# Kernel tuning notes

Measured on AMD Instinct MI355X. Metric: run time of the kernel, lower is better.

The kernel has to match this reference:

```python
import jax, jax.numpy as jnp
import numpy as np

LOG2PI = float(np.log(2.0 * np.pi))


def setup_inputs() -> dict:
    key = jax.random.key(0)
    k1, k2, k3 = jax.random.split(key, 3)
    N, D = 2048, 64
    z = jax.random.normal(k1, (N, D), dtype=jnp.float32)
    z_mean = jax.random.normal(k2, (N, D), dtype=jnp.float32)
    z_log_squared_scale = jax.random.normal(k3, (N, D), dtype=jnp.float32)
    return {"z": z, "z_mean": z_mean, "z_log_squared_scale": z_log_squared_scale}


def gaussian_log_density(samples, mean, log_var):
    # log N(samples; mean, exp(log_var)), elementwise per dim
    inv_var = jnp.exp(-log_var)
    diff = samples - mean
    return -0.5 * (diff * diff * inv_var + log_var + LOG2PI)


def reference(z, z_mean, z_log_squared_scale):
    # Pairwise log q(z_i | x_j) per latent dim: [N, N, D]
    log_qz_prob = gaussian_log_density(
        z[:, None, :], z_mean[None, :, :], z_log_squared_scale[None, :, :]
    )
    # sum_d logsumexp_j  -> log prod_d q(z_d)
    log_qz_product = jnp.sum(jax.scipy.special.logsumexp(log_qz_prob, axis=1), axis=1)
    # logsumexp_j sum_d  -> log q(z)
    log_qz = jax.scipy.special.logsumexp(jnp.sum(log_qz_prob, axis=2), axis=1)
    return jnp.mean(log_qz_product - log_qz)
```

## Files before the change

kernel.cpp:

```cpp
#include <hip/hip_runtime.h>
#include <hip/hip_fp16.h>
#include <math.h>
#include <stdint.h>

#define LOG2E  1.44269504088896340736f
#define LN2    0.69314718055994530942f
#define LOG2PI 1.8378770664093453f

#define NN 2048
#define DD 64

#define BIAS_F   16252928.0f
#define KBIT     2205910303u
#define CLAMP_LO 8388608.0f
#define CLAMP_HI 16777215.0f

#define C1250H 0x64E264E2u
#define KK16   0x63DC63DCu
#define SHL5   0x00050005u

typedef short          bf16x8 __attribute__((ext_vector_type(8)));
typedef float          f32x16 __attribute__((ext_vector_type(16)));

union PkU { uint32_t u; __half h[2]; };

__device__ __forceinline__ float fexp2(float x) { return __builtin_amdgcn_exp2f(x); }
__device__ __forceinline__ float flog2(float x) { return __builtin_amdgcn_logf(x); }
__device__ __forceinline__ unsigned short f2bf(float f) {
    uint32_t u = __float_as_uint(f);
    u += 0x7FFFu + ((u >> 16) & 1u);
    return (unsigned short)(u >> 16);
}
__device__ __forceinline__ float ubf(unsigned short s) {
    return __uint_as_float((uint32_t)s << 16);
}
__device__ __forceinline__ uint32_t bfpack(float a, float b) {
    return (uint32_t)f2bf(a) | ((uint32_t)f2bf(b) << 16);
}
__device__ __forceinline__ uint32_t h1(float x) {
    return (uint32_t)__half_as_ushort(__float2half_rn(x));
}
__device__ __forceinline__ uint32_t hdup(float x) { uint32_t t = h1(x); return t | (t << 16); }
__device__ __forceinline__ uint32_t hpack(float a, float b) { return h1(a) | (h1(b) << 16); }

__device__ __forceinline__ uint32_t pk_fma(uint32_t a, uint32_t b, uint32_t c) {
    uint32_t d;
    asm("v_pk_fma_f16 %0, %1, %2, %3" : "=v"(d) : "v"(a), "v"(b), "v"(c));
    return d;
}
__device__ __forceinline__ uint32_t pk_nfma(uint32_t a, uint32_t b, uint32_t c) {
    uint32_t d;
    asm("v_pk_fma_f16 %0, %1, %2, %3 neg_lo:[1,0,0] neg_hi:[1,0,0]"
        : "=v"(d) : "v"(a), "v"(b), "v"(c));
    return d;
}
__device__ __forceinline__ uint32_t pk_max(uint32_t a, uint32_t b) {
    uint32_t d;
    asm("v_pk_max_f16 %0, %1, %2" : "=v"(d) : "v"(a), "v"(b));
    return d;
}
__device__ __forceinline__ uint32_t pk_addf(uint32_t a, uint32_t b) {
    uint32_t d;
    asm("v_pk_add_f16 %0, %1, %2" : "=v"(d) : "v"(a), "v"(b));
    return d;
}
__device__ __forceinline__ uint32_t pk_shl(uint32_t a, uint32_t sh) {
    uint32_t d;
    asm("v_pk_lshlrev_b16 %0, %1, %2" : "=v"(d) : "v"(sh), "v"(a));
    return d;
}
__device__ __forceinline__ uint32_t pk_addu(uint32_t a, uint32_t b) {
    uint32_t d;
    asm("v_pk_add_u16 %0, %1, %2" : "=v"(d) : "v"(a), "v"(b));
    return d;
}

__global__ __launch_bounds__(256) void k1(
    const float* __restrict__ z, const float* __restrict__ zm,
    const float* __restrict__ zlv,
    uint4* __restrict__ smC4,
    uint32_t* __restrict__ pqfH, uint32_t* __restrict__ pqfL,
    uint32_t* __restrict__ zfH, uint32_t* __restrict__ zfL,
    float* __restrict__ CjS, uint32_t* __restrict__ zpkT)
{
    __shared__ float L[32][65];
    int tid = threadIdx.x, lane = tid & 63, row = tid >> 6;

    if (blockIdx.x < 128) {
        int jb = blockIdx.x * 16;
        #pragma unroll
        for (int c = 0; c < 4; ++c) {
            int j   = jb + c * 4 + row;
            int idx = j * DD + lane;
            float mean = zm[idx], lv = zlv[idx];
            float p   = -0.72134752f * fexp2(-lv * LOG2E);
            float q   = -2.0f * mean * p;
            float c22 = -0.72134752f * (lv + LOG2PI);
            float sp  = 5.65685424f * __builtin_sqrtf(-p);
            float msp = -mean * sp;
            float Cp  = fmaf(32.0f, c22, 1952.0f);
            smC4[idx] = make_uint4(hdup(sp), hdup(msp), hdup(Cp), 0u);
            unsigned short hp = f2bf(p), hq = f2bf(q);
            pqfH[idx] = (uint32_t)hp | ((uint32_t)hq << 16);
            pqfL[idx] = bfpack(p - ubf(hp), q - ubf(hq));
            float t = fmaf(mean * mean, p, c22);
            #pragma unroll
            for (int off = 32; off; off >>= 1) t += __shfl_xor(t, off, 64);
            if (lane == 0) CjS[j] = fmaf(t + 64.0f, 65536.0f, BIAS_F);
        }
    } else {
        int ib = (blockIdx.x - 128) * 32;
        #pragma unroll
        for (int c = 0; c < 8; ++c) {
            int il  = c * 4 + row;
            int idx = (ib + il) * DD + lane;
            float zv = z[idx];
            L[il][lane] = zv;
            float z2 = zv * zv;
            unsigned short hz2 = f2bf(z2), hz = f2bf(zv);
            zfH[idx] = (uint32_t)hz2 | ((uint32_t)hz << 16);
            zfL[idx] = bfpack(z2 - ubf(hz2), zv - ubf(hz));
        }
        __syncthreads();
        #pragma unroll
        for (int k = 0; k < 4; ++k) {
            int e = k * 256 + tid;
            int u = e & 7, d = (e >> 3) & 63, itl = e >> 9;
            float za = L[itl * 16 + 2 * u][d];
            float zb = L[itl * 16 + 2 * u + 1][d];
            zpkT[((ib >> 4) + itl) * 512 + d * 8 + u] = hpack(za, zb);
        }
    }
}

__global__ __launch_bounds__(256) void kw(
    const uint4* __restrict__ smC4, const uint32_t* __restrict__ zpkT,
    const uint32_t* __restrict__ zfH, const uint32_t* __restrict__ zfL,
    const uint32_t* __restrict__ pqfH, const uint32_t* __restrict__ pqfL,
    const float* __restrict__ CjS,
    __half* __restrict__ sums, float* __restrict__ k2part)
{
    __shared__ float shbuf[4096];
    int tid = threadIdx.x, lane = tid & 63, w = tid >> 6;

    if (blockIdx.x < 1024) {
        float (*sm)[16][64] = (float (*)[16][64])shbuf;
        int it = blockIdx.x >> 3, jsl = blockIdx.x & 7;
        int j0 = jsl * 256 + w * 64;

        uint32_t zpk[8], acc[8];
        #pragma unroll
        for (int u = 0; u < 8; ++u) {
            zpk[u] = zpkT[it * 512 + lane * 8 + u];
            acc[u] = 0u;
        }
        uint32_t kk = KK16, sh5 = SHL5, clf = C1250H;
        asm volatile("" : "+v"(kk), "+v"(sh5), "+v"(clf));

        const uint4* sp = smC4 + (size_t)j0 * DD + lane;
        #pragma unroll 4
        for (int jj = 0; jj < 64; ++jj) {
            uint4 v = sp[(size_t)jj * DD];
            #pragma unroll
            for (int u = 0; u < 8; ++u) {
                uint32_t wp = pk_fma(zpk[u], v.x, v.y);
                uint32_t y  = pk_nfma(wp, wp, v.z);
                y = pk_max(y, clf);
                uint32_t e = pk_addu(pk_shl(y, sh5), kk);
                acc[u] = pk_addf(acc[u], e);
            }
        }

        #pragma unroll
        for (int u = 0; u < 8; ++u) {
            PkU a; a.u = acc[u];
            sm[w][2 * u][lane]     = __half2float(a.h[0]);
            sm[w][2 * u + 1][lane] = __half2float(a.h[1]);
        }
        __syncthreads();
        #pragma unroll
        for (int k = 0; k < 4; ++k) {
            int e = k * 256 + tid;
            int il = e >> 6, d = e & 63;
            float v2 = sm[0][il][d] + sm[1][il][d] + sm[2][il][d] + sm[3][il][d];
            sums[((size_t)jsl * NN + it * 16 + il) * DD + d] =
                __float2half_rn(v2 * 0.0625f);
        }
    } else {
        float* cjsL = shbuf;
        for (int t = tid; t < NN; t += 256) cjsL[t] = CjS[t];
        __syncthreads();

        int gid = (blockIdx.x - 1024) * 4 + w;
        int it = gid >> 5, jg = gid & 31;
        int l31 = lane & 31, h = lane >> 5;

        const char* zbH = (const char*)zfH + (size_t)(it * 32 + l31) * 256 + h * 16;
        const char* zbL = (const char*)zfL + (size_t)(it * 32 + l31) * 256 + h * 16;
        bf16x8 BH[8], BL[8];
        #pragma unroll
        for (int kc = 0; kc < 8; ++kc) {
            BH[kc] = *(const bf16x8*)(zbH + kc * 32);
            BL[kc] = *(const bf16x8*)(zbL + kc * 32);
        }

        float isum = 0.0f;
        #pragma unroll
        for (int t4 = 0; t4 < 2; ++t4) {
            int jt = jg * 2 + t4;
            const char* abH = (const char*)pqfH + (size_t)(jt * 32 + l31) * 256 + h * 16;
            const char* abL = (const char*)pqfL + (size_t)(jt * 32 + l31) * 256 + h * 16;
            f32x16 acc;
            #pragma unroll
            for (int r = 0; r < 16; ++r) acc[r] = 0.0f;
            #pragma unroll
            for (int kc = 0; kc < 8; ++kc) {
                bf16x8 AH = *(const bf16x8*)(abH + kc * 32);
                bf16x8 AL = *(const bf16x8*)(abL + kc * 32);
                acc = __builtin_amdgcn_mfma_f32_32x32x16_bf16(AH, BH[kc], acc, 0, 0, 0);
                acc = __builtin_amdgcn_mfma_f32_32x32x16_bf16(AH, BL[kc], acc, 0, 0, 0);
                acc = __builtin_amdgcn_mfma_f32_32x32x16_bf16(AL, BH[kc], acc, 0, 0, 0);
            }
            #pragma unroll
            for (int r = 0; r < 16; ++r) {
                int R = (r & 3) + 8 * (r >> 2) + 4 * h;
                float y = fmaf(acc[r], 65536.0f, cjsL[jt * 32 + R]);
                y = fminf(fmaxf(y, CLAMP_LO), CLAMP_HI);
                isum += __uint_as_float((__float_as_uint(y) << 7) + KBIT);
            }
        }
        isum += __shfl_xor(isum, 32, 64);
        if (lane < 32) k2part[(size_t)jg * NN + it * 32 + l31] = isum;
    }
}

__global__ __launch_bounds__(256) void k5(
    const __half* __restrict__ sums, const float* __restrict__ k2part,
    float* __restrict__ diff)
{
    int lane = threadIdx.x & 63, w = threadIdx.x >> 6;
    int i = blockIdx.x * 4 + w;

    float tot = 0.0f;
    #pragma unroll
    for (int q = 0; q < 8; ++q)
        tot += __half2float(sums[((size_t)q * NN + i) * DD + lane]);
    float t = flog2(tot);
    #pragma unroll
    for (int off = 32; off; off >>= 1) t += __shfl_xor(t, off, 64);

    float s2 = (lane < 32) ? k2part[(size_t)lane * NN + i] : 0.0f;
    #pragma unroll
    for (int off = 32; off; off >>= 1) s2 += __shfl_xor(s2, off, 64);

    if (lane == 0) diff[i] = LN2 * (t - flog2(s2) - 128.0f);
}

__global__ __launch_bounds__(256) void k6(
    const float* __restrict__ diff, float* __restrict__ out)
{
    __shared__ float red[256];
    int tid = threadIdx.x;
    float t = 0.0f;
    for (int k = tid; k < NN; k += 256) t += diff[k];
    red[tid] = t;
    __syncthreads();
    #pragma unroll
    for (int off = 128; off; off >>= 1) {
        if (tid < off) red[tid] += red[tid + off];
        __syncthreads();
    }
    if (tid == 0) out[0] = red[0] * (1.0f / (float)NN);
}

extern "C" void kernel_launch(void* const* d_in, const int* in_sizes, int n_in,
                              void* d_out, int out_size, void* d_ws, size_t ws_size,
                              hipStream_t stream)
{
    const float* z   = (const float*)d_in[0];
    const float* zm  = (const float*)d_in[1];
    const float* zlv = (const float*)d_in[2];
    float* out = (float*)d_out;

    char* b = (char*)d_ws;
    uint4*    smC4 = (uint4*)(b);
    uint32_t* pqfH = (uint32_t*)(b + (2 << 20));
    uint32_t* pqfL = (uint32_t*)(b + (2 << 20) + (512 << 10));
    uint32_t* zfH  = (uint32_t*)(b + (3 << 20));
    uint32_t* zfL  = (uint32_t*)(b + (3 << 20) + (512 << 10));
    uint32_t* zpkT = (uint32_t*)(b + (4 << 20));
    float*    CjS  = (float*)(b + (4 << 20) + (256 << 10));
    __half*   sums = (__half*)(b + (5 << 20));
    float*    k2p  = (float*)(b + (7 << 20));
    float*    diff = (float*)(b + (7 << 20) + (256 << 10));

    k1<<<192,  256, 0, stream>>>(z, zm, zlv, smC4, pqfH, pqfL, zfH, zfL, CjS, zpkT);
    kw<<<1536, 256, 0, stream>>>(smC4, zpkT, zfH, zfL, pqfH, pqfL, CjS, sums, k2p);
    k5<<<512,  256, 0, stream>>>(sums, k2p, diff);
    k6<<<1,    256, 0, stream>>>(diff, out);
}
```

Baseline: 47.78 us.

## Pack per-j coefficients into uint2, widen kw blocks, and store packed half sums

```diff
diff --git a/kernel.cpp b/kernel.cpp
--- a/kernel.cpp
+++ b/kernel.cpp
@@ -18,6 +18,8 @@
 #define C1250H 0x64E264E2u
 #define KK16   0x63DC63DCu
 #define SHL5   0x00050005u
+#define SELA   0x01000100u
+#define SELB   0x03020302u
 
 typedef short          bf16x8 __attribute__((ext_vector_type(8)));
 typedef float          f32x16 __attribute__((ext_vector_type(16)));
@@ -74,11 +76,16 @@
     asm("v_pk_add_u16 %0, %1, %2" : "=v"(d) : "v"(a), "v"(b));
     return d;
 }
+__device__ __forceinline__ uint32_t perm(uint32_t src, uint32_t sel) {
+    uint32_t d;
+    asm("v_perm_b32 %0, %1, %2, %3" : "=v"(d) : "v"(src), "v"(src), "v"(sel));
+    return d;
+}
 
 __global__ __launch_bounds__(256) void k1(
     const float* __restrict__ z, const float* __restrict__ zm,
     const float* __restrict__ zlv,
-    uint4* __restrict__ smC4,
+    uint2* __restrict__ smC2,
     uint32_t* __restrict__ pqfH, uint32_t* __restrict__ pqfL,
     uint32_t* __restrict__ zfH, uint32_t* __restrict__ zfL,
     float* __restrict__ CjS, uint32_t* __restrict__ zpkT)
@@ -99,7 +106,7 @@
             float sp  = 5.65685424f * __builtin_sqrtf(-p);
             float msp = -mean * sp;
             float Cp  = fmaf(32.0f, c22, 1952.0f);
-            smC4[idx] = make_uint4(hdup(sp), hdup(msp), hdup(Cp), 0u);
+            smC2[idx] = make_uint2(hpack(sp, msp), hdup(Cp));
             unsigned short hp = f2bf(p), hq = f2bf(q);
             pqfH[idx] = (uint32_t)hp | ((uint32_t)hq << 16);
             pqfL[idx] = bfpack(p - ubf(hp), q - ubf(hq));
@@ -133,20 +140,19 @@
     }
 }
 
-__global__ __launch_bounds__(256) void kw(
-    const uint4* __restrict__ smC4, const uint32_t* __restrict__ zpkT,
+__global__ __launch_bounds__(512) void kw(
+    const uint2* __restrict__ smC2, const uint32_t* __restrict__ zpkT,
     const uint32_t* __restrict__ zfH, const uint32_t* __restrict__ zfL,
     const uint32_t* __restrict__ pqfH, const uint32_t* __restrict__ pqfL,
     const float* __restrict__ CjS,
-    __half* __restrict__ sums, float* __restrict__ k2part)
-{
-    __shared__ float shbuf[4096];
+    uint32_t* __restrict__ sums, float* __restrict__ k2part)
+{
+    __shared__ float shbuf[2048];
     int tid = threadIdx.x, lane = tid & 63, w = tid >> 6;
 
-    if (blockIdx.x < 1024) {
-        float (*sm)[16][64] = (float (*)[16][64])shbuf;
-        int it = blockIdx.x >> 3, jsl = blockIdx.x & 7;
-        int j0 = jsl * 256 + w * 64;
+    if (blockIdx.x < 512) {
+        int it = blockIdx.x >> 2, jsl = blockIdx.x & 3;
+        int j0 = jsl * 512 + (w & 3) * 64 + (w >> 2) * 256;
 
         uint32_t zpk[8], acc[8];
         #pragma unroll
@@ -154,44 +160,50 @@
             zpk[u] = zpkT[it * 512 + lane * 8 + u];
             acc[u] = 0u;
         }
-        uint32_t kk = KK16, sh5 = SHL5, clf = C1250H;
-        asm volatile("" : "+v"(kk), "+v"(sh5), "+v"(clf));
-
-        const uint4* sp = smC4 + (size_t)j0 * DD + lane;
+        uint32_t kk = KK16, sh5 = SHL5, clf = C1250H, sA = SELA, sB = SELB;
+        asm volatile("" : "+v"(kk), "+v"(sh5), "+v"(clf), "+v"(sA), "+v"(sB));
+
+        const uint2* sp2 = smC2 + (size_t)j0 * DD + lane;
         #pragma unroll 4
         for (int jj = 0; jj < 64; ++jj) {
-            uint4 v = sp[(size_t)jj * DD];
+            uint2 v = sp2[(size_t)jj * DD];
+            uint32_t sd = perm(v.x, sA);
+            uint32_t md = perm(v.x, sB);
             #pragma unroll
             for (int u = 0; u < 8; ++u) {
-                uint32_t wp = pk_fma(zpk[u], v.x, v.y);
-                uint32_t y  = pk_nfma(wp, wp, v.z);
+                uint32_t wp = pk_fma(zpk[u], sd, md);
+                uint32_t y  = pk_nfma(wp, wp, v.y);
                 y = pk_max(y, clf);
                 uint32_t e = pk_addu(pk_shl(y, sh5), kk);
                 acc[u] = pk_addf(acc[u], e);
             }
         }
 
-        #pragma unroll
-        for (int u = 0; u < 8; ++u) {
-            PkU a; a.u = acc[u];
-            sm[w][2 * u][lane]     = __half2float(a.h[0]);
-            sm[w][2 * u + 1][lane] = __half2float(a.h[1]);
+        uint32_t* sl = (uint32_t*)shbuf;
+        if (w < 4) {
+            #pragma unroll
+            for (int u = 0; u < 8; ++u) sl[(w * 8 + u) * 64 + lane] = acc[u];
         }
         __syncthreads();
-        #pragma unroll
-        for (int k = 0; k < 4; ++k) {
-            int e = k * 256 + tid;
-            int il = e >> 6, d = e & 63;
-            float v2 = sm[0][il][d] + sm[1][il][d] + sm[2][il][d] + sm[3][il][d];
-            sums[((size_t)jsl * NN + it * 16 + il) * DD + d] =
-                __float2half_rn(v2 * 0.0625f);
+        if (w >= 4) {
+            int slice = jsl * 4 + (w - 4);
+            #pragma unroll
+            for (int u = 0; u < 8; ++u) {
+                PkU a, b;
+                a.u = acc[u];
+                b.u = sl[((w - 4) * 8 + u) * 64 + lane];
+                float lo = __half2float(a.h[0]) + __half2float(b.h[0]);
+                float hi = __half2float(a.h[1]) + __half2float(b.h[1]);
+                sums[((size_t)slice * 1024 + it * 8 + u) * 64 + lane] =
+                    hpack(lo * 0.0625f, hi * 0.0625f);
+            }
         }
     } else {
         float* cjsL = shbuf;
-        for (int t = tid; t < NN; t += 256) cjsL[t] = CjS[t];
+        for (int t = tid; t < NN; t += 512) cjsL[t] = CjS[t];
         __syncthreads();
 
-        int gid = (blockIdx.x - 1024) * 4 + w;
+        int gid = (blockIdx.x - 512) * 8 + w;
         int it = gid >> 5, jg = gid & 31;
         int l31 = lane & 31, h = lane >> 5;
 
@@ -240,11 +252,12 @@
 {
     int lane = threadIdx.x & 63, w = threadIdx.x >> 6;
     int i = blockIdx.x * 4 + w;
+    int ip = i >> 1, hsel = i & 1;
 
     float tot = 0.0f;
     #pragma unroll
-    for (int q = 0; q < 8; ++q)
-        tot += __half2float(sums[((size_t)q * NN + i) * DD + lane]);
+    for (int q = 0; q < 16; ++q)
+        tot += __half2float(sums[(((size_t)q * 1024 + ip) * 64 + lane) * 2 + hsel]);
     float t = flog2(tot);
     #pragma unroll
     for (int off = 32; off; off >>= 1) t += __shfl_xor(t, off, 64);
@@ -283,19 +296,19 @@
     float* out = (float*)d_out;
 
     char* b = (char*)d_ws;
-    uint4*    smC4 = (uint4*)(b);
-    uint32_t* pqfH = (uint32_t*)(b + (2 << 20));
-    uint32_t* pqfL = (uint32_t*)(b + (2 << 20) + (512 << 10));
-    uint32_t* zfH  = (uint32_t*)(b + (3 << 20));
-    uint32_t* zfL  = (uint32_t*)(b + (3 << 20) + (512 << 10));
-    uint32_t* zpkT = (uint32_t*)(b + (4 << 20));
-    float*    CjS  = (float*)(b + (4 << 20) + (256 << 10));
-    __half*   sums = (__half*)(b + (5 << 20));
-    float*    k2p  = (float*)(b + (7 << 20));
-    float*    diff = (float*)(b + (7 << 20) + (256 << 10));
-
-    k1<<<192,  256, 0, stream>>>(z, zm, zlv, smC4, pqfH, pqfL, zfH, zfL, CjS, zpkT);
-    kw<<<1536, 256, 0, stream>>>(smC4, zpkT, zfH, zfL, pqfH, pqfL, CjS, sums, k2p);
-    k5<<<512,  256, 0, stream>>>(sums, k2p, diff);
-    k6<<<1,    256, 0, stream>>>(diff, out);
-}
+    uint2*    smC2 = (uint2*)(b);
+    uint32_t* pqfH = (uint32_t*)(b + (1 << 20));
+    uint32_t* pqfL = (uint32_t*)(b + (1 << 20) + (512 << 10));
+    uint32_t* zfH  = (uint32_t*)(b + (2 << 20));
+    uint32_t* zfL  = (uint32_t*)(b + (2 << 20) + (512 << 10));
+    uint32_t* zpkT = (uint32_t*)(b + (3 << 20));
+    float*    CjS  = (float*)(b + (3 << 20) + (256 << 10));
+    uint32_t* sums = (uint32_t*)(b + (3 << 20) + (512 << 10));
+    float*    k2p  = (float*)(b + (7 << 20) + (512 << 10));
+    float*    diff = (float*)(b + (7 << 20) + (768 << 10));
+
+    k1<<<192, 256, 0, stream>>>(z, zm, zlv, smC2, pqfH, pqfL, zfH, zfL, CjS, zpkT);
+    kw<<<768, 512, 0, stream>>>(smC2, zpkT, zfH, zfL, pqfH, pqfL, CjS, sums, k2p);
+    k5<<<512, 256, 0, stream>>>((const __half*)sums, k2p, diff);
+    k6<<<1,   256, 0, stream>>>(diff, out);
+}
```

After: 51.71 us. 1.08x slower.
